# Kernel tuning notes

Measured on AMD Instinct MI355X. Metric: run time of the kernel, lower is better.

## Reference

```python
import jax, jax.numpy as jnp
import numpy as np

D_MODEL = 1024
N_HEADS = 16
HEAD_DIM = 64
D_FF = 4096


def rmsnorm(x, w):
    eps = jnp.finfo(x.dtype).eps
    var = jnp.mean(jnp.square(x), axis=-1, keepdims=True)
    return x * jax.lax.rsqrt(var + eps) * w


def setup_inputs() -> dict:
    key = jax.random.key(0)
    ks = jax.random.split(key, 8)
    d, h, hd, dff = D_MODEL, N_HEADS, HEAD_DIM, D_FF
    s = 0.02
    return {
        "x": jax.random.normal(ks[0], (2, 2048, d), dtype=jnp.float32),
        "norm_w": jnp.ones((d,), dtype=jnp.float32),
        "Wq": jax.random.normal(ks[1], (d, h * hd), dtype=jnp.float32) * s,
        "Wk": jax.random.normal(ks[2], (d, h * hd), dtype=jnp.float32) * s,
        "Wv": jax.random.normal(ks[3], (d, h * hd), dtype=jnp.float32) * s,
        "Wo": jax.random.normal(ks[4], (h * hd, d), dtype=jnp.float32) * s,
        "W1": jax.random.normal(ks[5], (d, dff), dtype=jnp.float32) * s,
        "W2": jax.random.normal(ks[6], (dff, d), dtype=jnp.float32) * s,
    }


def reference(x, norm_w, Wq, Wk, Wv, Wo, W1, W2):
    B, T, d = x.shape
    h, hd = N_HEADS, HEAD_DIM
    scale = 1.0 / np.sqrt(hd)

    xn = rmsnorm(x, norm_w)

    # attention branch
    q = (xn @ Wq).reshape(B, T, h, hd).transpose(0, 2, 1, 3)  # [B,h,T,hd]
    k = (xn @ Wk).reshape(B, T, h, hd).transpose(0, 2, 1, 3)
    v = (xn @ Wv).reshape(B, T, h, hd).transpose(0, 2, 1, 3)
    attn = jnp.einsum("bhqd,bhkd->bhqk", q, k) * scale
    causal = jnp.tril(jnp.ones((T, T), dtype=bool))
    attn = jnp.where(causal, attn, -jnp.inf)
    attn = jax.nn.softmax(attn, axis=-1)
    out = jnp.einsum("bhqk,bhkd->bhqd", attn, v)
    out = out.transpose(0, 2, 1, 3).reshape(B, T, h * hd)
    attn_out = out @ Wo

    # FFN branch
    ffn_out = jax.nn.silu(xn @ W1) @ W2

    return x + attn_out + ffn_out
```

## Files before the change

### kernel.cpp

```cpp
#include <hip/hip_runtime.h>

#define DM   1024
#define DFF  4096
#define NH   16
#define HD   64
#define TT   2048
#define BT   4096
#define KC   5120

typedef unsigned short u16;
typedef unsigned int   u32;
typedef __attribute__((ext_vector_type(8))) short s16x8;
typedef __attribute__((ext_vector_type(4))) float f32x4;

__device__ __forceinline__ u16 f2bf(float f) {
  u32 u = __builtin_bit_cast(u32, f);
  u += 0x7fffu + ((u >> 16) & 1u);
  return (u16)(u >> 16);
}

__device__ __forceinline__ void gl2lds16(const void* g, void* l) {
  __builtin_amdgcn_global_load_lds((__attribute__((address_space(1))) void*)(g),
                                   (__attribute__((address_space(3))) void*)(l),
                                   16, 0, 0);
}

#define S_BARRIER() do { __builtin_amdgcn_s_barrier(); __builtin_amdgcn_sched_barrier(0); } while (0)
#define VMWAIT(n)   asm volatile("s_waitcnt vmcnt(" #n ")" ::: "memory")

__global__ __launch_bounds__(256) void rmsnorm_k(const float* __restrict__ x,
                                                 const float* __restrict__ w,
                                                 u16* __restrict__ xn) {
  const int row = blockIdx.x;
  const int t = threadIdx.x;
  const float4 v = ((const float4*)(x + (size_t)row * DM))[t];
  float ss = v.x*v.x + v.y*v.y + v.z*v.z + v.w*v.w;
  #pragma unroll
  for (int off = 32; off; off >>= 1) ss += __shfl_xor(ss, off, 64);
  __shared__ float red[4];
  if ((t & 63) == 0) red[t >> 6] = ss;
  __syncthreads();
  const float tot = red[0] + red[1] + red[2] + red[3];
  const float r = __builtin_amdgcn_rsqf(tot * (1.0f / DM) + 1.1920929e-7f);
  const float4 wv = ((const float4*)w)[t];
  u16* o = xn + (size_t)row * DM + t * 4;
  o[0] = f2bf(v.x * r * wv.x);
  o[1] = f2bf(v.y * r * wv.y);
  o[2] = f2bf(v.z * r * wv.z);
  o[3] = f2bf(v.w * r * wv.w);
}

__global__ __launch_bounds__(256) void wtrans_k(const float* __restrict__ W,
                                                u16* __restrict__ Wt,
                                                int K, int N, int pitch, int koff) {
  __shared__ float tile[32][33];
  const int n0 = blockIdx.x * 32, k0 = blockIdx.y * 32;
  const int tx = threadIdx.x, ty = threadIdx.y;
  #pragma unroll
  for (int i = 0; i < 4; ++i)
    tile[ty + i*8][tx] = W[(size_t)(k0 + ty + i*8) * N + n0 + tx];
  __syncthreads();
  #pragma unroll
  for (int i = 0; i < 4; ++i)
    Wt[(size_t)(n0 + ty + i*8) * pitch + koff + k0 + tx] = f2bf(tile[tx][ty + i*8]);
}

__global__ __launch_bounds__(512, 2) void gemm_fused(const u16* __restrict__ A,
                                                     const u16* __restrict__ Bt,
                                                     u16* __restrict__ qkb,
                                                     u16* __restrict__ vtg,
                                                     u16* __restrict__ acat) {
  const int K = 1024;
  __shared__ u16 sA[2 * 16384];
  __shared__ u16 sB[2 * 16384];
  const int t = threadIdx.x;
  const int lane = t & 63, wave = t >> 6;
  const int quad = lane >> 4, l4 = lane & 15;
  const int wy = wave >> 2, wx = wave & 3;
  const size_t mBase = (size_t)blockIdx.y * 256;
  const size_t nBase = (size_t)blockIdx.x * 256;

  const int grow = t >> 3;
  const int gchk = ((t & 7) ^ (grow & 7)) * 8;
  const u16* AgR = A  + (mBase + grow) * K + gchk;
  const u16* BgR = Bt + (nBase + grow) * K + gchk;
  char* dA = (char*)sA;
  char* dB = (char*)sB;
  const int woff = wave * 1024;

  const int cs0 = ((quad)     ^ (l4 & 7)) * 8;
  const int cs1 = ((4 + quad) ^ (l4 & 7)) * 8;

  f32x4 acc[8][4];
  #pragma unroll
  for (int i = 0; i < 8; ++i)
    #pragma unroll
    for (int j = 0; j < 4; ++j)
      acc[i][j] = (f32x4)0.0f;

  s16x8 a[4][2], b[4][2];

  #define STG(p, slot, kt) do {                                                  \
    const int k0_ = (kt) * 64;                                                   \
    if ((p) == 0) {                                                              \
      gl2lds16(BgR + (size_t)0*64*K + k0_, dB + (slot)*32768 +     0 + woff);    \
      gl2lds16(BgR + (size_t)1*64*K + k0_, dB + (slot)*32768 +  8192 + woff);    \
    } else if ((p) == 1) {                                                       \
      gl2lds16(BgR + (size_t)2*64*K + k0_, dB + (slot)*32768 + 16384 + woff);    \
      gl2lds16(BgR + (size_t)3*64*K + k0_, dB + (slot)*32768 + 24576 + woff);    \
    } else if ((p) == 2) {                                                       \
      gl2lds16(AgR + (size_t)0*64*K + k0_, dA + (slot)*32768 +     0 + woff);    \
      gl2lds16(AgR + (size_t)2*64*K + k0_, dA + (slot)*32768 + 16384 + woff);    \
    } else {                                                                     \
      gl2lds16(AgR + (size_t)1*64*K + k0_, dA + (slot)*32768 +  8192 + woff);    \
      gl2lds16(AgR + (size_t)3*64*K + k0_, dA + (slot)*32768 + 24576 + woff);    \
    }                                                                            \
  } while (0)

  #define RDA(slot, qm) do {                                                     \
    const u16* p_ = sA + (slot)*16384 + wy*8192;                                 \
    _Pragma("unroll")                                                            \
    for (int m_ = 0; m_ < 4; ++m_) {                                             \
      const int ro_ = (((qm)*4 + m_)*16 + l4) * 64;                              \
      a[m_][0] = *(const s16x8*)&p_[ro_ + cs0];                                  \
      a[m_][1] = *(const s16x8*)&p_[ro_ + cs1];                                  \
    }                                                                            \
  } while (0)

  #define RDB(slot, qn) do {                                                     \
    const u16* p_ = sB + (slot)*16384 + (wx>>1)*8192 + (wx&1)*4096;              \
    _Pragma("unroll")                                                            \
    for (int n_ = 0; n_ < 2; ++n_) {                                             \
      const int ro_ = (((qn)*2 + n_)*16 + l4) * 64;                              \
      b[(qn)*2 + n_][0] = *(const s16x8*)&p_[ro_ + cs0];                         \
      b[(qn)*2 + n_][1] = *(const s16x8*)&p_[ro_ + cs1];                         \
    }                                                                            \
  } while (0)

  #define MM(qm, qn) do {                                                        \
    __builtin_amdgcn_s_setprio(1);                                               \
    _Pragma("unroll")                                                            \
    for (int m_ = 0; m_ < 4; ++m_)                                               \
      _Pragma("unroll")                                                          \
      for (int n_ = 0; n_ < 2; ++n_) {                                           \
        acc[(qm)*4+m_][(qn)*2+n_] = __builtin_amdgcn_mfma_f32_16x16x32_bf16(     \
            a[m_][0], b[(qn)*2+n_][0], acc[(qm)*4+m_][(qn)*2+n_], 0, 0, 0);      \
        acc[(qm)*4+m_][(qn)*2+n_] = __builtin_amdgcn_mfma_f32_16x16x32_bf16(     \
            a[m_][1], b[(qn)*2+n_][1], acc[(qm)*4+m_][(qn)*2+n_], 0, 0, 0);      \
      }                                                                          \
    __builtin_amdgcn_s_setprio(0);                                               \
  } while (0)

  STG(0, 0, 0); STG(1, 0, 0); STG(2, 0, 0); STG(3, 0, 0);
  VMWAIT(2);
  S_BARRIER();

  for (int i = 0; i < 7; ++i) {
    const int kt1 = 2*i + 1, kt2 = 2*i + 2;
    RDA(0,0); RDB(0,0); STG(0,1,kt1); S_BARRIER(); MM(0,0);            S_BARRIER();
    RDB(0,1);           STG(1,1,kt1); S_BARRIER(); MM(0,1); VMWAIT(4); S_BARRIER();
    RDA(0,1);           STG(2,1,kt1); S_BARRIER(); MM(1,0);            S_BARRIER();
                        STG(3,1,kt1); S_BARRIER(); MM(1,1); VMWAIT(2); S_BARRIER();
    RDA(1,0); RDB(1,0); STG(0,0,kt2); S_BARRIER(); MM(0,0);            S_BARRIER();
    RDB(1,1);           STG(1,0,kt2); S_BARRIER(); MM(0,1); VMWAIT(4); S_BARRIER();
    RDA(1,1);           STG(2,0,kt2); S_BARRIER(); MM(1,0);            S_BARRIER();
                        STG(3,0,kt2); S_BARRIER(); MM(1,1); VMWAIT(2); S_BARRIER();
  }
  RDA(0,0); RDB(0,0); STG(0,1,15); S_BARRIER(); MM(0,0);            S_BARRIER();
  RDB(0,1);           STG(1,1,15); S_BARRIER(); MM(0,1); VMWAIT(4); S_BARRIER();
  RDA(0,1);           STG(2,1,15); S_BARRIER(); MM(1,0);            S_BARRIER();
                      STG(3,1,15); S_BARRIER(); MM(1,1); VMWAIT(2); S_BARRIER();
  RDA(1,0); RDB(1,0);              S_BARRIER(); MM(0,0);            S_BARRIER();
  RDB(1,1);                        S_BARRIER(); MM(0,1); VMWAIT(0); S_BARRIER();
  RDA(1,1);                        S_BARRIER(); MM(1,0);            S_BARRIER();
                                   S_BARRIER(); MM(1,1);            S_BARRIER();

  #undef STG
  #undef RDA
  #undef RDB
  #undef MM

  #pragma unroll
  for (int i = 0; i < 8; ++i) {
    const size_t row0 = mBase + wy*128 + i*16 + quad*4;
    #pragma unroll
    for (int j = 0; j < 4; ++j) {
      const int col = (int)nBase + wx*64 + j*16 + l4;
      if (nBase < 1024) {
        #pragma unroll
        for (int rg = 0; rg < 4; ++rg)
          qkb[(row0 + rg) * 2048 + col] = f2bf(acc[i][j][rg] * 0.18033688011f);
      } else if (nBase < 2048) {
        #pragma unroll
        for (int rg = 0; rg < 4; ++rg)
          qkb[(row0 + rg) * 2048 + col] = f2bf(acc[i][j][rg]);
      } else if (nBase < 3072) {
        const int cv = col - 2048, hh = cv >> 6, dd = cv & 63;
        const int bb = (int)(row0 >> 11), t0 = (int)(row0 & 2047);
        ushort4 pk;
        pk.x = f2bf(acc[i][j][0]); pk.y = f2bf(acc[i][j][1]);
        pk.z = f2bf(acc[i][j][2]); pk.w = f2bf(acc[i][j][3]);
        *(ushort4*)(vtg + ((size_t)((bb*16 + hh)*64 + dd)) * 2048 + t0) = pk;
      } else {
        #pragma unroll
        for (int rg = 0; rg < 4; ++rg) {
          float v = acc[i][j][rg];
          v = v / (1.0f + __expf(-v));
          acat[(row0 + rg) * (size_t)KC + 1024 + (col - 3072)] = f2bf(v);
        }
      }
    }
  }
}

__global__ __launch_bounds__(256, 2) void gemm_final(const u16* __restrict__ A,
                                                     const u16* __restrict__ Bt,
                                                     const float* __restrict__ x,
                                                     float* __restrict__ out) {
  __shared__ u16 sA[4 * 64 * 32];
  __shared__ u16 sB[4 * 128 * 32];
  const int t = threadIdx.x;
  const int lane = t & 63, wave = t >> 6;
  const int quad = lane >> 4, l4 = lane & 15;
  const int wy = wave >> 1, wx = wave & 1;
  const size_t mBase = (size_t)blockIdx.y * 64;
  const size_t nBase = (size_t)blockIdx.x * 128;
  const int r  = t >> 2;
  const int c8 = ((t & 3) ^ ((t >> 3) & 3)) * 8;
  const int qsw = (quad ^ ((l4 >> 1) & 3)) * 8;
  const u16* Ag  = A  + (mBase + r) * KC + c8;
  const u16* Bg0 = Bt + (nBase + r) * KC + c8;
  const u16* Bg1 = Bg0 + (size_t)64 * KC;
  char* sAb = (char*)sA + (wave << 10);
  char* sBb = (char*)sB + (wave << 10);

  f32x4 acc[2][4];
  #pragma unroll
  for (int i = 0; i < 2; ++i)
    #pragma unroll
    for (int j = 0; j < 4; ++j)
      acc[i][j] = (f32x4)0.0f;

  auto issue = [&](int bf, int k0) {
    gl2lds16(Ag  + k0, sAb + bf*4096);
    gl2lds16(Bg0 + k0, sBb + bf*8192);
    gl2lds16(Bg1 + k0, sBb + bf*8192 + 4096);
  };

  auto compute = [&](int bf) {
    const u16* pA = sA + bf * 2048;
    const u16* pB = sB + bf * 4096;
    s16x8 af[2], bfr[4];
    #pragma unroll
    for (int i = 0; i < 2; ++i)
      af[i] = *(const s16x8*)&pA[(wy*32 + i*16 + l4) * 32 + qsw];
    #pragma unroll
    for (int j = 0; j < 4; ++j)
      bfr[j] = *(const s16x8*)&pB[(wx*64 + j*16 + l4) * 32 + qsw];
    #pragma unroll
    for (int i = 0; i < 2; ++i)
      #pragma unroll
      for (int j = 0; j < 4; ++j)
        acc[i][j] = __builtin_amdgcn_mfma_f32_16x16x32_bf16(af[i], bfr[j], acc[i][j], 0, 0, 0);
  };

  const int NIT = KC / 32;
  issue(0, 0); issue(1, 32); issue(2, 64);
  for (int kt = 0; kt < NIT - 2; ++kt) {
    VMWAIT(6);
    S_BARRIER();
    if (kt + 3 < NIT) issue((kt + 3) & 3, (kt + 3) * 32);
    compute(kt & 3);
  }
  VMWAIT(3); S_BARRIER(); compute((NIT - 2) & 3);
  VMWAIT(0); S_BARRIER(); compute((NIT - 1) & 3);

  #pragma unroll
  for (int i = 0; i < 2; ++i) {
    const size_t row0 = mBase + wy*32 + i*16 + quad*4;
    #pragma unroll
    for (int j = 0; j < 4; ++j) {
      const int col = (int)nBase + wx*64 + j*16 + l4;
      #pragma unroll
      for (int rg = 0; rg < 4; ++rg) {
        const size_t idx = (row0 + rg) * (size_t)DM + col;
        out[idx] = x[idx] + acc[i][j][rg];
      }
    }
  }
}

__global__ __launch_bounds__(128) void attn_k(const u16* __restrict__ qk,
                                              const u16* __restrict__ vtg,
                                              u16* __restrict__ acat) {
  const int bh = blockIdx.x, b = bh >> 4, h = bh & 15;
  const int qt = 63 - blockIdx.y;
  const int qw = qt * 32;
  const int wave = threadIdx.x >> 6, lane = threadIdx.x & 63;
  const int quad = lane >> 4, l4 = lane & 15;
  const u16* Qp = qk + (size_t)b * TT * 2048 + h * HD;
  const u16* Kp = Qp + 1024;
  const u16* Vp = vtg + (size_t)bh * 64 * 2048;

  __shared__ u16 Pb[2][32][72];
  __shared__ float Ob[32][68];
  __shared__ float Lb[32];

  s16x8 qf[2][2];
  #pragma unroll
  for (int mi = 0; mi < 2; ++mi)
    #pragma unroll
    for (int kf = 0; kf < 2; ++kf)
      qf[mi][kf] = *(const s16x8*)(Qp + (size_t)(qw + mi*16 + l4) * 2048 + kf*32 + quad*8);

  const s16x8 ones = {0x3F80,0x3F80,0x3F80,0x3F80,0x3F80,0x3F80,0x3F80,0x3F80};

  f32x4 o[2][4];
  f32x4 lacc[2];
  #pragma unroll
  for (int mi = 0; mi < 2; ++mi) {
    lacc[mi] = (f32x4)0.0f;
    #pragma unroll
    for (int ni = 0; ni < 4; ++ni) o[mi][ni] = (f32x4)0.0f;
  }

  const int n   = (qt + 2) >> 1;
  const int n0  = (n + 1) >> 1;
  const int kt0 = wave ? n0 : 0;
  const int kt1 = wave ? n : n0;

  for (int kt = kt0; kt < kt1; ++kt) {
    const int k0 = kt * 64;

    f32x4 st[4][2];
    #pragma unroll
    for (int nj = 0; nj < 4; ++nj) {
      const u16* kr = Kp + (size_t)(k0 + nj*16 + l4) * 2048 + quad*8;
      const s16x8 kf0 = *(const s16x8*)kr;
      const s16x8 kf1 = *(const s16x8*)(kr + 32);
      #pragma unroll
      for (int mi = 0; mi < 2; ++mi) {
        f32x4 a = (f32x4)0.0f;
        a = __builtin_amdgcn_mfma_f32_16x16x32_bf16(kf0, qf[mi][0], a, 0, 0, 0);
        a = __builtin_amdgcn_mfma_f32_16x16x32_bf16(kf1, qf[mi][1], a, 0, 0, 0);
        st[nj][mi] = a;
      }
    }

    s16x8 vb[2][4];
    #pragma unroll
    for (int kf2 = 0; kf2 < 2; ++kf2)
      #pragma unroll
      for (int ni = 0; ni < 4; ++ni)
        vb[kf2][ni] = *(const s16x8*)(Vp + (size_t)(ni*16 + l4) * 2048 + k0 + kf2*32 + quad*8);

    if (k0 + 63 > qw) {
      #pragma unroll
      for (int nj = 0; nj < 4; ++nj)
        #pragma unroll
        for (int mi = 0; mi < 2; ++mi)
          #pragma unroll
          for (int rg = 0; rg < 4; ++rg) {
            const int key = k0 + nj*16 + quad*4 + rg;
            const int q   = qw + mi*16 + l4;
            if (key > q) st[nj][mi][rg] = -1e30f;
          }
    }

    #pragma unroll
    for (int nj = 0; nj < 4; ++nj)
      #pragma unroll
      for (int mi = 0; mi < 2; ++mi) {
        float p0 = __builtin_amdgcn_exp2f(st[nj][mi][0]);
        float p1 = __builtin_amdgcn_exp2f(st[nj][mi][1]);
        float p2 = __builtin_amdgcn_exp2f(st[nj][mi][2]);
        float p3 = __builtin_amdgcn_exp2f(st[nj][mi][3]);
        uint2 w;
        w.x = __builtin_amdgcn_perm(__builtin_bit_cast(u32, p1),
                                    __builtin_bit_cast(u32, p0), 0x07060302u);
        w.y = __builtin_amdgcn_perm(__builtin_bit_cast(u32, p3),
                                    __builtin_bit_cast(u32, p2), 0x07060302u);
        *(uint2*)&Pb[wave][mi*16 + l4][nj*16 + quad*4] = w;
      }

    #pragma unroll
    for (int kf2 = 0; kf2 < 2; ++kf2) {
      s16x8 pa[2];
      #pragma unroll
      for (int mi = 0; mi < 2; ++mi)
        pa[mi] = *(const s16x8*)&Pb[wave][mi*16 + l4][kf2*32 + quad*8];
      #pragma unroll
      for (int mi = 0; mi < 2; ++mi) {
        lacc[mi] = __builtin_amdgcn_mfma_f32_16x16x32_bf16(pa[mi], ones, lacc[mi], 0, 0, 0);
        #pragma unroll
        for (int ni = 0; ni < 4; ++ni)
          o[mi][ni] = __builtin_amdgcn_mfma_f32_16x16x32_bf16(pa[mi], vb[kf2][ni], o[mi][ni], 0, 0, 0);
      }
    }
  }

  if (wave == 1) {
    #pragma unroll
    for (int mi = 0; mi < 2; ++mi)
      #pragma unroll
      for (int rg = 0; rg < 4; ++rg) {
        const int row = mi*16 + quad*4 + rg;
        #pragma unroll
        for (int ni = 0; ni < 4; ++ni) Ob[row][ni*16 + l4] = o[mi][ni][rg];
        if (l4 == 0) Lb[row] = lacc[mi][rg];
      }
  }
  __syncthreads();
  if (wave == 0) {
    #pragma unroll
    for (int mi = 0; mi < 2; ++mi)
      #pragma unroll
      for (int rg = 0; rg < 4; ++rg) {
        const int row = mi*16 + quad*4 + rg;
        const float inv = 1.0f / (lacc[mi][rg] + Lb[row]);
        #pragma unroll
        for (int ni = 0; ni < 4; ++ni)
          Pb[0][row][ni*16 + l4] = f2bf((o[mi][ni][rg] + Ob[row][ni*16 + l4]) * inv);
      }
    #pragma unroll
    for (int it = 0; it < 4; ++it) {
      const int row = it*8 + (lane >> 3);
      const int c0  = (lane & 7) * 8;
      const s16x8 pk = *(const s16x8*)&Pb[0][row][c0];
      *(s16x8*)(acat + ((size_t)b * TT + qw + row) * KC + h*HD + c0) = pk;
    }
  }
}

extern "C" void kernel_launch(void* const* d_in, const int* in_sizes, int n_in,
                              void* d_out, int out_size, void* d_ws, size_t ws_size,
                              hipStream_t stream) {
  (void)in_sizes; (void)n_in; (void)out_size; (void)ws_size;
  const float* x  = (const float*)d_in[0];
  const float* nw = (const float*)d_in[1];
  const float* Wq = (const float*)d_in[2];
  const float* Wk = (const float*)d_in[3];
  const float* Wv = (const float*)d_in[4];
  const float* Wo = (const float*)d_in[5];
  const float* W1 = (const float*)d_in[6];
  const float* W2 = (const float*)d_in[7];

  char* ws = (char*)d_ws;
  u16*   xn      = (u16*)(ws);
  u16*   wqkv1_t = (u16*)(ws + ((size_t)8  << 20));
  u16*   bcat    = (u16*)(ws + ((size_t)22 << 20));
  u16*   qkb     = (u16*)(ws + ((size_t)32 << 20));
  u16*   vtg     = (u16*)(ws + ((size_t)48 << 20));
  u16*   acat    = (u16*)(ws + ((size_t)56 << 20));
  float* dout    = (float*)d_out;

  rmsnorm_k<<<BT, 256, 0, stream>>>(x, nw, xn);
  const dim3 tb(32, 8);
  wtrans_k<<<dim3(32, 32),  tb, 0, stream>>>(Wq, wqkv1_t,                      1024, 1024, 1024, 0);
  wtrans_k<<<dim3(32, 32),  tb, 0, stream>>>(Wk, wqkv1_t + (size_t)1024*1024,  1024, 1024, 1024, 0);
  wtrans_k<<<dim3(32, 32),  tb, 0, stream>>>(Wv, wqkv1_t + (size_t)2048*1024,  1024, 1024, 1024, 0);
  wtrans_k<<<dim3(128, 32), tb, 0, stream>>>(W1, wqkv1_t + (size_t)3072*1024,  1024, 4096, 1024, 0);
  wtrans_k<<<dim3(32, 32),  tb, 0, stream>>>(Wo, bcat,                         1024, 1024, 5120, 0);
  wtrans_k<<<dim3(32, 128), tb, 0, stream>>>(W2, bcat,                         4096, 1024, 5120, 1024);

  gemm_fused<<<dim3(28, 16), 512, 0, stream>>>(xn, wqkv1_t, qkb, vtg, acat);
  attn_k<<<dim3(32, 64), 128, 0, stream>>>(qkb, vtg, acat);
  gemm_final<<<dim3(8, 64), 256, 0, stream>>>(acat, bcat, x, dout);
}
```

Baseline: 361.6 us.

## Deepen final GEMM pipeline to six stages and swizzle block order for L2 reuse

The final GEMM goes from a 4-slot, 3-in-flight global-to-LDS ring to a 6-slot ring with five loads in flight, adjusting the vmcnt waits and drain sequence to match. Both GEMM kernels remap block indices so consecutive workgroups cover different tiles, grouping the ones that share A or B panels to improve L2/MALL locality. The deeper buffering raises LDS use per block from 48KB to 72KB, which may limit how many blocks fit on a CU.

```diff
diff --git a/kernel.cpp b/kernel.cpp
--- a/kernel.cpp
+++ b/kernel.cpp
@@ -77,8 +77,11 @@
   const int lane = t & 63, wave = t >> 6;
   const int quad = lane >> 4, l4 = lane & 15;
   const int wy = wave >> 2, wx = wave & 3;
-  const size_t mBase = (size_t)blockIdx.y * 256;
-  const size_t nBase = (size_t)blockIdx.x * 256;
+  const int d  = blockIdx.x + blockIdx.y * 28;
+  const int vv = (d & 7) * 56 + (d >> 3);
+  const int bxs = vv % 28, bys = vv / 28;
+  const size_t mBase = (size_t)bys * 256;
+  const size_t nBase = (size_t)bxs * 256;
 
   const int grow = t >> 3;
   const int gchk = ((t & 7) ^ (grow & 7)) * 8;
@@ -217,14 +220,17 @@
                                                      const u16* __restrict__ Bt,
                                                      const float* __restrict__ x,
                                                      float* __restrict__ out) {
-  __shared__ u16 sA[4 * 64 * 32];
-  __shared__ u16 sB[4 * 128 * 32];
+  __shared__ u16 sA[6 * 64 * 32];
+  __shared__ u16 sB[6 * 128 * 32];
   const int t = threadIdx.x;
   const int lane = t & 63, wave = t >> 6;
   const int quad = lane >> 4, l4 = lane & 15;
   const int wy = wave >> 1, wx = wave & 1;
-  const size_t mBase = (size_t)blockIdx.y * 64;
-  const size_t nBase = (size_t)blockIdx.x * 128;
+  const int d  = blockIdx.x + (blockIdx.y << 3);
+  const int vb = ((d & 7) << 6) | (d >> 3);
+  const int bx = vb & 7, by = vb >> 3;
+  const size_t mBase = (size_t)by * 64;
+  const size_t nBase = (size_t)bx * 128;
   const int r  = t >> 2;
   const int c8 = ((t & 3) ^ ((t >> 3) & 3)) * 8;
   const int qsw = (quad ^ ((l4 >> 1) & 3)) * 8;
@@ -241,15 +247,15 @@
     for (int j = 0; j < 4; ++j)
       acc[i][j] = (f32x4)0.0f;
 
-  auto issue = [&](int bf, int k0) {
-    gl2lds16(Ag  + k0, sAb + bf*4096);
-    gl2lds16(Bg0 + k0, sBb + bf*8192);
-    gl2lds16(Bg1 + k0, sBb + bf*8192 + 4096);
+  auto issue = [&](int sl, int k0) {
+    gl2lds16(Ag  + k0, sAb + sl*4096);
+    gl2lds16(Bg0 + k0, sBb + sl*8192);
+    gl2lds16(Bg1 + k0, sBb + sl*8192 + 4096);
   };
 
-  auto compute = [&](int bf) {
-    const u16* pA = sA + bf * 2048;
-    const u16* pB = sB + bf * 4096;
+  auto compute = [&](int sl) {
+    const u16* pA = sA + sl * 2048;
+    const u16* pB = sB + sl * 4096;
     s16x8 af[2], bfr[4];
     #pragma unroll
     for (int i = 0; i < 2; ++i)
@@ -265,15 +271,20 @@
   };
 
   const int NIT = KC / 32;
-  issue(0, 0); issue(1, 32); issue(2, 64);
-  for (int kt = 0; kt < NIT - 2; ++kt) {
-    VMWAIT(6);
+  issue(0, 0); issue(1, 32); issue(2, 64); issue(3, 96); issue(4, 128);
+  int sl = 0;
+  for (int kt = 0; kt < NIT - 5; ++kt) {
+    VMWAIT(12);
     S_BARRIER();
-    if (kt + 3 < NIT) issue((kt + 3) & 3, (kt + 3) * 32);
-    compute(kt & 3);
-  }
-  VMWAIT(3); S_BARRIER(); compute((NIT - 2) & 3);
-  VMWAIT(0); S_BARRIER(); compute((NIT - 1) & 3);
+    issue(sl == 0 ? 5 : sl - 1, (kt + 5) * 32);
+    compute(sl);
+    sl = (sl == 5) ? 0 : sl + 1;
+  }
+  VMWAIT(12); S_BARRIER(); compute(sl); sl = (sl == 5) ? 0 : sl + 1;
+  VMWAIT(9);  S_BARRIER(); compute(sl); sl = (sl == 5) ? 0 : sl + 1;
+  VMWAIT(6);  S_BARRIER(); compute(sl); sl = (sl == 5) ? 0 : sl + 1;
+  VMWAIT(3);  S_BARRIER(); compute(sl); sl = (sl == 5) ? 0 : sl + 1;
+  VMWAIT(0);  S_BARRIER(); compute(sl);
 
   #pragma unroll
   for (int i = 0; i < 2; ++i) {
```

New measurement: 367.7 us. About the same (+1.7%).
